# Kernel optimization log

Measured on AMD Instinct MI355X. Metric: run time of the kernel, lower is better.

Reference implementation:

```python
import jax, jax.numpy as jnp
import numpy as np

SIZE = 2.0            # scene extent, matches init size
N_LEVELS = 16         # Instant-NGP default
TABLE_SIZE = 1 << 19  # hash entries per level (power of 2)
FEAT = 2              # embedding_length per level
BASE_RES = 16         # init resolution
MAX_RES = 2048
N_POINTS = 1 << 21

_OFFS = np.array([[(c >> d) & 1 for d in range(3)] for c in range(8)])  # [8,3] corner bits
_PRIMES = np.array([1, 2654435761, 805459861], dtype=np.uint32)         # NGP spatial hash primes


def setup_inputs() -> dict:
    key = jax.random.key(0)
    k1, k2 = jax.random.split(key)
    xyz = (jax.random.uniform(k1, (N_POINTS, 3), dtype=jnp.float32) - 0.5) * SIZE
    tables = jax.random.normal(k2, (N_LEVELS, TABLE_SIZE, FEAT), dtype=jnp.float32) * 1e-2
    # geometric resolution schedule 16 -> 2048 over 16 levels
    growth = (MAX_RES / BASE_RES) ** (np.arange(N_LEVELS) / (N_LEVELS - 1))
    resolutions = jnp.asarray(np.floor(BASE_RES * growth).astype(np.int32))
    return {"xyz": xyz, "tables": tables, "resolutions": resolutions}


def _encode(xyz, tables, resolutions):
    u = xyz / SIZE + 0.5                              # [N,3] in [0,1)
    offs_u = jnp.asarray(_OFFS.astype(np.uint32))     # [8,3]
    offs_f = jnp.asarray(_OFFS.astype(np.float32))    # [8,3]
    primes = jnp.asarray(_PRIMES)

    def level(_, xs):
        table, res = xs                               # [T,F], scalar int32
        p = u * res.astype(jnp.float32)               # [N,3]
        p0 = jnp.floor(p)
        w = p - p0                                    # trilinear fractions [N,3]
        c = p0.astype(jnp.uint32)[:, None, :] + offs_u[None]     # [N,8,3]
        h = (c[..., 0] * primes[0]) ^ (c[..., 1] * primes[1]) ^ (c[..., 2] * primes[2])
        idx = (h & jnp.uint32(TABLE_SIZE - 1)).astype(jnp.int32)  # [N,8]
        feats = table[idx]                                        # [N,8,F] gather
        wc = jnp.prod(jnp.where(offs_f[None] > 0, w[:, None, :], 1.0 - w[:, None, :]), axis=-1)  # [N,8]
        return None, jnp.sum(feats * wc[..., None], axis=1)      # [N,F]

    _, embs = jax.lax.scan(level, None, (tables, resolutions))   # [L,N,F]
    n = xyz.shape[0]
    return jnp.transpose(embs, (1, 0, 2)).reshape(n, N_LEVELS * FEAT)


def reference(xyz, tables, resolutions):
    return _encode(xyz, tables, resolutions)
```

## Files before the change

kernel.cpp:

```cpp
#include <hip/hip_runtime.h>
#include <hip/hip_fp16.h>

#define NLV 16
#define TBL (1u << 19)
#define TMASK (TBL - 1u)
#define P1 2654435761u
#define P2 805459861u

typedef float vf2 __attribute__((ext_vector_type(2)));
typedef float vf4 __attribute__((ext_vector_type(4)));
typedef unsigned vu2 __attribute__((ext_vector_type(2)));
typedef unsigned vu4 __attribute__((ext_vector_type(4)));

__device__ __forceinline__ vf2 h2_to_f2(unsigned bits) {
    union { unsigned u; __half2 h; } c; c.u = bits;
    float2 f = __half22float2(c.h);
    vf2 r; r.x = f.x; r.y = f.y; return r;
}
__device__ __forceinline__ unsigned f2_to_h2(float a, float b) {
    union { __half2 h; unsigned u; } c; c.h = __floats2half2_rn(a, b);
    return c.u;
}

__global__ __launch_bounds__(256) void convert_tables(
    const float* __restrict__ tables, unsigned* __restrict__ htab, int total)
{
    int i = blockIdx.x * 256 + threadIdx.x;
    int e0 = i * 2;
    if (e0 >= total) return;
    vf4 v = *(const vf4*)(tables + (size_t)e0 * 2);
    vu2 o; o.x = f2_to_h2(v.x, v.y); o.y = f2_to_h2(v.z, v.w);
    *(vu2*)(htab + e0) = o;
}

__global__ __launch_bounds__(256) void ngp_gather_h(
    const float* __restrict__ xyz,
    const unsigned* __restrict__ htab,
    const int* __restrict__ resolutions,
    unsigned* __restrict__ wsout,
    int n, int nbPerLevel)
{
    int L = blockIdx.x / nbPerLevel;
    int chunk = blockIdx.x % nbPerLevel;
    int p0 = chunk * 512 + (int)threadIdx.x;

    float res = (float)resolutions[L];
    const unsigned* __restrict__ tab = htab + (size_t)L * TBL;
    unsigned* __restrict__ wl = wsout + (size_t)L * n;

#pragma unroll
    for (int q = 0; q < 2; ++q) {
        int p = p0 + q * 256;
        if (p >= n) continue;

        float x = xyz[(size_t)p * 3 + 0];
        float y = xyz[(size_t)p * 3 + 1];
        float z = xyz[(size_t)p * 3 + 2];
        float ux = x * 0.5f + 0.5f;
        float uy = y * 0.5f + 0.5f;
        float uz = z * 0.5f + 0.5f;
        float px = ux * res, py = uy * res, pz = uz * res;
        float fx = floorf(px), fy = floorf(py), fz = floorf(pz);
        float wx = px - fx, wy = py - fy, wz = pz - fz;
        unsigned cx = (unsigned)fx, cy = (unsigned)fy, cz = (unsigned)fz;
        float vx = 1.0f - wx, vy = 1.0f - wy, vz = 1.0f - wz;

        unsigned e = cx & ~1u;
        unsigned odd = cx & 1u;
        unsigned hy0 = cy * P1, hy1 = hy0 + P1;
        unsigned hz0 = cz * P2, hz1 = hz0 + P2;

        unsigned R[4];
        R[0] = hy0 ^ hz0; R[1] = hy1 ^ hz0;
        R[2] = hy0 ^ hz1; R[3] = hy1 ^ hz1;
        float wyz[4];
        wyz[0] = vy * vz; wyz[1] = wy * vz;
        wyz[2] = vy * wz; wyz[3] = wy * wz;

        vu2 dA[4]; unsigned selA[4];
#pragma unroll
        for (int j = 0; j < 4; ++j) {
            unsigned idx = (e ^ R[j]) & TMASK;
            selA[j] = idx & 1u;
            dA[j] = *(const vu2*)(tab + (idx & ~1u));
        }
        vu2 dB[4] = {}; unsigned selB[4] = {};
        if (odd) {
#pragma unroll
            for (int j = 0; j < 4; ++j) {
                unsigned idx = ((e + 2u) ^ R[j]) & TMASK;
                selB[j] = idx & 1u;
                dB[j] = *(const vu2*)(tab + (idx & ~1u));
            }
        }

        float a0 = 0.0f, a1 = 0.0f;
#pragma unroll
        for (int j = 0; j < 4; ++j) {
            unsigned s0 = selA[j] ^ odd;
            unsigned b0 = s0 ? dA[j].y : dA[j].x;
            unsigned fromA = selA[j] ? dA[j].x : dA[j].y;
            unsigned fromB = selB[j] ? dB[j].y : dB[j].x;
            unsigned b1 = odd ? fromB : fromA;
            vf2 f0 = h2_to_f2(b0);
            vf2 f1 = h2_to_f2(b1);
            float W0 = wyz[j] * vx;
            float W1 = wyz[j] * wx;
            a0 += f0.x * W0; a0 += f1.x * W1;
            a1 += f0.y * W0; a1 += f1.y * W1;
        }
        wl[p] = f2_to_h2(a0, a1);
    }
}

__global__ __launch_bounds__(256) void ngp_transpose_h(
    const unsigned* __restrict__ ws,
    float* __restrict__ out, int n)
{
    int t = blockIdx.x * 256 + threadIdx.x;
    int p = t * 4;
    if (p >= n) return;

    if (p + 3 < n && (n & 3) == 0) {
        vu4 m[NLV];
#pragma unroll
        for (int L = 0; L < NLV; ++L)
            m[L] = *(const vu4*)(ws + (size_t)L * n + p);
#pragma unroll
        for (int pt = 0; pt < 4; ++pt) {
            vf4* o = (vf4*)(out + (size_t)(p + pt) * (NLV * 2));
#pragma unroll
            for (int i = 0; i < 8; ++i) {
                unsigned ba = pt == 0 ? m[2 * i].x : pt == 1 ? m[2 * i].y
                             : pt == 2 ? m[2 * i].z : m[2 * i].w;
                unsigned bb = pt == 0 ? m[2 * i + 1].x : pt == 1 ? m[2 * i + 1].y
                             : pt == 2 ? m[2 * i + 1].z : m[2 * i + 1].w;
                vf2 ga = h2_to_f2(ba), gb = h2_to_f2(bb);
                vf4 r; r.x = ga.x; r.y = ga.y; r.z = gb.x; r.w = gb.y;
                o[i] = r;
            }
        }
    } else {
        for (int pt = 0; pt < 4 && p + pt < n; ++pt) {
            vf4* o = (vf4*)(out + (size_t)(p + pt) * (NLV * 2));
#pragma unroll
            for (int i = 0; i < 8; ++i) {
                vf2 ga = h2_to_f2(ws[(size_t)(2 * i) * n + p + pt]);
                vf2 gb = h2_to_f2(ws[(size_t)(2 * i + 1) * n + p + pt]);
                vf4 r; r.x = ga.x; r.y = ga.y; r.z = gb.x; r.w = gb.y;
                o[i] = r;
            }
        }
    }
}

__global__ __launch_bounds__(256) void ngp_encode_kernel(
    const float* __restrict__ xyz,
    const float* __restrict__ tables,
    const int* __restrict__ resolutions,
    float* __restrict__ out,
    int n)
{
    int p = blockIdx.x * blockDim.x + threadIdx.x;
    if (p >= n) return;

    float x = xyz[(size_t)p * 3 + 0];
    float y = xyz[(size_t)p * 3 + 1];
    float z = xyz[(size_t)p * 3 + 2];
    float ux = x * 0.5f + 0.5f;
    float uy = y * 0.5f + 0.5f;
    float uz = z * 0.5f + 0.5f;

    float acc[NLV * 2];

#pragma unroll
    for (int L = 0; L < NLV; ++L) {
        float res = (float)resolutions[L];
        float px = ux * res, py = uy * res, pz = uz * res;
        float fx = floorf(px), fy = floorf(py), fz = floorf(pz);
        float wx = px - fx, wy = py - fy, wz = pz - fz;
        unsigned cx = (unsigned)fx, cy = (unsigned)fy, cz = (unsigned)fz;
        unsigned hx0 = cx, hx1 = cx + 1u;
        unsigned hy0 = cy * P1, hy1 = hy0 + P1;
        unsigned hz0 = cz * P2, hz1 = hz0 + P2;
        const vf2* __restrict__ tab = (const vf2*)tables + (size_t)L * TBL;
        float vx = 1.0f - wx, vy = 1.0f - wy, vz = 1.0f - wz;
        float a0 = 0.0f, a1 = 0.0f;
#pragma unroll
        for (int c = 0; c < 8; ++c) {
            unsigned h = ((c & 1) ? hx1 : hx0) ^
                         ((c & 2) ? hy1 : hy0) ^
                         ((c & 4) ? hz1 : hz0);
            vf2 f = tab[h & TMASK];
            float w = ((c & 1) ? wx : vx) *
                      ((c & 2) ? wy : vy) *
                      ((c & 4) ? wz : vz);
            a0 += f.x * w;
            a1 += f.y * w;
        }
        acc[L * 2 + 0] = a0;
        acc[L * 2 + 1] = a1;
    }

    vf4* o = (vf4*)(out + (size_t)p * (NLV * 2));
#pragma unroll
    for (int i = 0; i < 8; ++i) {
        vf4 r; r.x = acc[i * 4 + 0]; r.y = acc[i * 4 + 1];
        r.z = acc[i * 4 + 2]; r.w = acc[i * 4 + 3];
        o[i] = r;
    }
}

extern "C" void kernel_launch(void* const* d_in, const int* in_sizes, int n_in,
                              void* d_out, int out_size, void* d_ws, size_t ws_size,
                              hipStream_t stream) {
    const float* xyz = (const float*)d_in[0];
    const float* tables = (const float*)d_in[1];
    const int* resolutions = (const int*)d_in[2];
    float* out = (float*)d_out;

    int n = in_sizes[0] / 3;
    const int totalEntries = NLV * (int)TBL;
    const size_t tabBytes = (size_t)totalEntries * 4;
    const size_t wsoutBytes = (size_t)NLV * (size_t)n * 4;

    if (ws_size >= tabBytes + wsoutBytes) {
        unsigned* htab = (unsigned*)d_ws;
        unsigned* wsout = (unsigned*)((char*)d_ws + tabBytes);

        int gridC = (totalEntries / 2 + 255) / 256;
        hipLaunchKernelGGL(convert_tables, dim3(gridC), dim3(256), 0, stream,
                           tables, htab, totalEntries);

        int nbPerLevel = (n + 511) / 512;
        int grid1 = NLV * nbPerLevel;
        hipLaunchKernelGGL(ngp_gather_h, dim3(grid1), dim3(256), 0, stream,
                           xyz, htab, resolutions, wsout, n, nbPerLevel);

        int grid2 = ((n + 3) / 4 + 255) / 256;
        hipLaunchKernelGGL(ngp_transpose_h, dim3(grid2), dim3(256), 0, stream,
                           wsout, out, n);
    } else {
        int grid = (n + 255) / 256;
        hipLaunchKernelGGL(ngp_encode_kernel, dim3(grid), dim3(256), 0, stream,
                           xyz, tables, resolutions, out, n);
    }
}
```

Measured before the change: 886.4 us.

## Prepack normalized coords to float4 and batch four points per thread for gather MLP

Adds a small kernel that writes normalized xyz as aligned float4 to the workspace, so each gather level does one 16-byte load instead of three strided scalar loads. The gather kernel now handles four points per thread and issues all table loads for every point before any blending, which puts more independent random loads in flight per thread. The cost is an extra launch, 32 MB of extra workspace traffic, and higher register use that may lower occupancy.

```diff
diff --git a/kernel.cpp b/kernel.cpp
--- a/kernel.cpp
+++ b/kernel.cpp
@@ -33,8 +33,21 @@
     *(vu2*)(htab + e0) = o;
 }
 
+__global__ __launch_bounds__(256) void pack_u4(
+    const float* __restrict__ xyz, vf4* __restrict__ u4, int n)
+{
+    int p = blockIdx.x * 256 + threadIdx.x;
+    if (p >= n) return;
+    float x = xyz[(size_t)p * 3 + 0];
+    float y = xyz[(size_t)p * 3 + 1];
+    float z = xyz[(size_t)p * 3 + 2];
+    vf4 r; r.x = x * 0.5f + 0.5f; r.y = y * 0.5f + 0.5f;
+    r.z = z * 0.5f + 0.5f; r.w = 0.0f;
+    u4[p] = r;
+}
+
 __global__ __launch_bounds__(256) void ngp_gather_h(
-    const float* __restrict__ xyz,
+    const vf4* __restrict__ u4,
     const unsigned* __restrict__ htab,
     const int* __restrict__ resolutions,
     unsigned* __restrict__ wsout,
@@ -42,74 +55,83 @@
 {
     int L = blockIdx.x / nbPerLevel;
     int chunk = blockIdx.x % nbPerLevel;
-    int p0 = chunk * 512 + (int)threadIdx.x;
+    int p0 = chunk * 1024 + (int)threadIdx.x;
 
     float res = (float)resolutions[L];
     const unsigned* __restrict__ tab = htab + (size_t)L * TBL;
     unsigned* __restrict__ wl = wsout + (size_t)L * n;
 
-#pragma unroll
-    for (int q = 0; q < 2; ++q) {
+    unsigned Rj[4][4];
+    unsigned e[4], odd[4];
+    float wx[4], wyz[4][4];
+    bool valid[4];
+
+#pragma unroll
+    for (int q = 0; q < 4; ++q) {
         int p = p0 + q * 256;
-        if (p >= n) continue;
-
-        float x = xyz[(size_t)p * 3 + 0];
-        float y = xyz[(size_t)p * 3 + 1];
-        float z = xyz[(size_t)p * 3 + 2];
-        float ux = x * 0.5f + 0.5f;
-        float uy = y * 0.5f + 0.5f;
-        float uz = z * 0.5f + 0.5f;
-        float px = ux * res, py = uy * res, pz = uz * res;
+        valid[q] = (p < n);
+        int pp = valid[q] ? p : 0;
+        vf4 u = u4[pp];
+        float px = u.x * res, py = u.y * res, pz = u.z * res;
         float fx = floorf(px), fy = floorf(py), fz = floorf(pz);
-        float wx = px - fx, wy = py - fy, wz = pz - fz;
+        float wxl = px - fx, wyl = py - fy, wzl = pz - fz;
         unsigned cx = (unsigned)fx, cy = (unsigned)fy, cz = (unsigned)fz;
-        float vx = 1.0f - wx, vy = 1.0f - wy, vz = 1.0f - wz;
-
-        unsigned e = cx & ~1u;
-        unsigned odd = cx & 1u;
+        e[q] = cx & ~1u;
+        odd[q] = cx & 1u;
         unsigned hy0 = cy * P1, hy1 = hy0 + P1;
         unsigned hz0 = cz * P2, hz1 = hz0 + P2;
-
-        unsigned R[4];
-        R[0] = hy0 ^ hz0; R[1] = hy1 ^ hz0;
-        R[2] = hy0 ^ hz1; R[3] = hy1 ^ hz1;
-        float wyz[4];
-        wyz[0] = vy * vz; wyz[1] = wy * vz;
-        wyz[2] = vy * wz; wyz[3] = wy * wz;
-
-        vu2 dA[4]; unsigned selA[4];
+        Rj[q][0] = hy0 ^ hz0; Rj[q][1] = hy1 ^ hz0;
+        Rj[q][2] = hy0 ^ hz1; Rj[q][3] = hy1 ^ hz1;
+        float vy = 1.0f - wyl, vz = 1.0f - wzl;
+        wx[q] = wxl;
+        wyz[q][0] = vy * vz; wyz[q][1] = wyl * vz;
+        wyz[q][2] = vy * wzl; wyz[q][3] = wyl * wzl;
+    }
+
+    vu2 dA[4][4];
+#pragma unroll
+    for (int q = 0; q < 4; ++q)
 #pragma unroll
         for (int j = 0; j < 4; ++j) {
-            unsigned idx = (e ^ R[j]) & TMASK;
-            selA[j] = idx & 1u;
-            dA[j] = *(const vu2*)(tab + (idx & ~1u));
-        }
-        vu2 dB[4] = {}; unsigned selB[4] = {};
-        if (odd) {
+            unsigned idx = (e[q] ^ Rj[q][j]) & TMASK;
+            dA[q][j] = *(const vu2*)(tab + (idx & ~1u));
+        }
+
+    vu2 dB[4][4];
+#pragma unroll
+    for (int q = 0; q < 4; ++q) {
+#pragma unroll
+        for (int j = 0; j < 4; ++j) { dB[q][j].x = 0u; dB[q][j].y = 0u; }
+        if (odd[q]) {
 #pragma unroll
             for (int j = 0; j < 4; ++j) {
-                unsigned idx = ((e + 2u) ^ R[j]) & TMASK;
-                selB[j] = idx & 1u;
-                dB[j] = *(const vu2*)(tab + (idx & ~1u));
+                unsigned idx = ((e[q] + 2u) ^ Rj[q][j]) & TMASK;
+                dB[q][j] = *(const vu2*)(tab + (idx & ~1u));
             }
         }
-
+    }
+
+#pragma unroll
+    for (int q = 0; q < 4; ++q) {
+        float vx = 1.0f - wx[q];
         float a0 = 0.0f, a1 = 0.0f;
 #pragma unroll
         for (int j = 0; j < 4; ++j) {
-            unsigned s0 = selA[j] ^ odd;
-            unsigned b0 = s0 ? dA[j].y : dA[j].x;
-            unsigned fromA = selA[j] ? dA[j].x : dA[j].y;
-            unsigned fromB = selB[j] ? dB[j].y : dB[j].x;
-            unsigned b1 = odd ? fromB : fromA;
+            unsigned sA = Rj[q][j] & 1u;
+            unsigned s0 = sA ^ odd[q];
+            unsigned b0 = s0 ? dA[q][j].y : dA[q][j].x;
+            unsigned fromA = sA ? dA[q][j].x : dA[q][j].y;
+            unsigned fromB = sA ? dB[q][j].y : dB[q][j].x;
+            unsigned b1 = odd[q] ? fromB : fromA;
             vf2 f0 = h2_to_f2(b0);
             vf2 f1 = h2_to_f2(b1);
-            float W0 = wyz[j] * vx;
-            float W1 = wyz[j] * wx;
+            float W0 = wyz[q][j] * vx;
+            float W1 = wyz[q][j] * wx[q];
             a0 += f0.x * W0; a0 += f1.x * W1;
             a1 += f0.y * W0; a1 += f1.y * W1;
         }
-        wl[p] = f2_to_h2(a0, a1);
+        int p = p0 + q * 256;
+        if (valid[q]) wl[p] = f2_to_h2(a0, a1);
     }
 }
 
@@ -222,20 +244,26 @@
     int n = in_sizes[0] / 3;
     const int totalEntries = NLV * (int)TBL;
     const size_t tabBytes = (size_t)totalEntries * 4;
+    const size_t u4Bytes = (size_t)n * sizeof(vf4);
     const size_t wsoutBytes = (size_t)NLV * (size_t)n * 4;
 
-    if (ws_size >= tabBytes + wsoutBytes) {
+    if (ws_size >= tabBytes + u4Bytes + wsoutBytes) {
         unsigned* htab = (unsigned*)d_ws;
-        unsigned* wsout = (unsigned*)((char*)d_ws + tabBytes);
+        vf4* u4 = (vf4*)((char*)d_ws + tabBytes);
+        unsigned* wsout = (unsigned*)((char*)d_ws + tabBytes + u4Bytes);
 
         int gridC = (totalEntries / 2 + 255) / 256;
         hipLaunchKernelGGL(convert_tables, dim3(gridC), dim3(256), 0, stream,
                            tables, htab, totalEntries);
 
-        int nbPerLevel = (n + 511) / 512;
+        int gridU = (n + 255) / 256;
+        hipLaunchKernelGGL(pack_u4, dim3(gridU), dim3(256), 0, stream,
+                           xyz, u4, n);
+
+        int nbPerLevel = (n + 1023) / 1024;
         int grid1 = NLV * nbPerLevel;
         hipLaunchKernelGGL(ngp_gather_h, dim3(grid1), dim3(256), 0, stream,
-                           xyz, htab, resolutions, wsout, n, nbPerLevel);
+                           u4, htab, resolutions, wsout, n, nbPerLevel);
 
         int grid2 = ((n + 3) / 4 + 255) / 256;
         hipLaunchKernelGGL(ngp_transpose_h, dim3(grid2), dim3(256), 0, stream,
```

Result: no change. 898.4 us (+1.4%).
